# Kernel optimization log

Measured on AMD Instinct MI355X. Metric: run time of the kernel, lower is better.

## Reference

```python
import jax, jax.numpy as jnp
import numpy as np

EPS = 1e-6
NUM_HEADS = 12


def setup_inputs() -> dict:
    key = jax.random.key(0)
    k1, k2, k3, k4 = jax.random.split(key, 4)
    B, N, C = 8, 1024, 768
    x = jax.random.normal(k1, (B, N, C), dtype=jnp.float32)
    # random-walk visitation mask (nonnegative, row 'start_node' weights)
    mask = jax.random.uniform(k2, (N, N), dtype=jnp.float32)
    w_qkv = jax.random.normal(k3, (C, 3 * C), dtype=jnp.float32) * (C ** -0.5)
    w_out = jax.random.normal(k4, (C, C), dtype=jnp.float32) * (C ** -0.5)
    b_out = jnp.zeros((C,), dtype=jnp.float32)
    return {"x": x, "mask": mask, "w_qkv": w_qkv, "w_out": w_out, "b_out": b_out}


def reference(x, mask, w_qkv, w_out, b_out):
    B, N, C = x.shape
    H = NUM_HEADS
    D = C // H
    qkv = x @ w_qkv                      # [B, N, 3C]
    q, k, v = jnp.split(qkv, 3, axis=-1)
    # [B, N, C] -> [B, H, N, D]
    to_heads = lambda t: t.reshape(B, N, H, D).transpose(0, 2, 1, 3)
    q, k, v = to_heads(q), to_heads(k), to_heads(v)
    # feature map: relu + eps
    q = jax.nn.relu(q) + EPS
    k = jax.nn.relu(k) + EPS
    # graph smoothing: (q^T @ mask)^T  ==  einsum over the token axis
    q_graph = jnp.einsum('bhnd,nm->bhmd', q, mask)
    k_graph = jnp.einsum('bhnd,nm->bhmd', k, mask)
    q = q + 0.1 * q_graph
    k = k + 0.1 * k_graph
    # exact linear kernel, masked by random-walk mask
    linear_kernel = jnp.einsum('bhnd,bhmd->bhnm', q, k)   # [B, H, N, N]
    masked_kernel = linear_kernel * mask[None, None]
    z = 1.0 / (masked_kernel.sum(axis=-1, keepdims=True) + EPS)
    out = jnp.einsum('bhnm,bhmd->bhnd', masked_kernel, v) * z
    out = out.transpose(0, 2, 1, 3).reshape(B, N, C)
    return out @ w_out + b_out
```

## Files before the change

kernel.cpp:

```cpp
#include <hip/hip_runtime.h>


typedef unsigned short u16;
typedef unsigned int u32;
typedef __attribute__((ext_vector_type(8))) short short8;
typedef __attribute__((ext_vector_type(4))) float f32x4;

#define MFMA(a, b, c) __builtin_amdgcn_mfma_f32_16x16x32_bf16((a), (b), (c), 0, 0, 0)

__device__ __forceinline__ u16 f2b(float f) {
    unsigned u = __builtin_bit_cast(unsigned, f);
    return (u16)((u + 0x7FFFu + ((u >> 16) & 1u)) >> 16);
}
__device__ __forceinline__ float b2f(u16 h) {
    unsigned u = ((unsigned)h) << 16;
    return __builtin_bit_cast(float, u);
}
__device__ __forceinline__ void gl_lds16(const u16* g, u16* l) {
    __builtin_amdgcn_global_load_lds(
        (const __attribute__((address_space(1))) u32*)g,
        (__attribute__((address_space(3))) u32*)l, 16, 0, 0);
}

__global__ __launch_bounds__(256) void k_conv(const float* __restrict__ in,
                                              u16* __restrict__ out, int n) {
    int i = (blockIdx.x * 256 + threadIdx.x) * 4;
    if (i + 3 < n) {
        float4 v = *reinterpret_cast<const float4*>(&in[i]);
        ushort4 o;
        o.x = f2b(v.x); o.y = f2b(v.y); o.z = f2b(v.z); o.w = f2b(v.w);
        *reinterpret_cast<ushort4*>(&out[i]) = o;
    }
}

__global__ __launch_bounds__(256) void k_transconv(const float* __restrict__ in,
                                                   u16* __restrict__ out,
                                                   int R, int Cc, float alpha, float delta) {
    __shared__ float t[32][33];
    const int tx = threadIdx.x & 31, ty = threadIdx.x >> 5;
    const int r0 = blockIdx.y * 32, c0 = blockIdx.x * 32;
#pragma unroll
    for (int k = 0; k < 4; ++k)
        t[ty + 8 * k][tx] = in[(long)(r0 + ty + 8 * k) * Cc + c0 + tx];
    __syncthreads();
#pragma unroll
    for (int k = 0; k < 4; ++k) {
        const int c = c0 + ty + 8 * k, r = r0 + tx;
        float v = t[tx][ty + 8 * k] * alpha + ((r == c) ? delta : 0.f);
        out[(long)c * R + r] = f2b(v);
    }
}

template <int MODE>
__global__ __launch_bounds__(256) void k_gemm(const u16* __restrict__ A,
                                              const u16* __restrict__ Bm,
                                              void* __restrict__ Cv,
                                              const float* __restrict__ bias,
                                              int M, int N, int K,
                                              int lda, int ldb, int ldc,
                                              long boffB, long boffC) {
    __shared__ u16 As[128][40];
    __shared__ u16 Bs[128][40];
    const int tid = threadIdx.x;
    const int lane = tid & 63, wid = tid >> 6;
    const int lo = lane & 15, hi = lane >> 4;
    const int wr = wid >> 1, wc = wid & 1;
    const int m0 = blockIdx.y * 128, n0 = blockIdx.x * 128;
    const u16* Bz = Bm + (long)blockIdx.z * boffB;
    const int srow = tid >> 1, skoff = (tid & 1) * 16;
    const u16* Ag = A + (long)(m0 + srow) * lda + skoff;
    const u16* Bg = Bz + (long)(n0 + srow) * ldb + skoff;

    f32x4 acc[4][4] = {};
    for (int k0 = 0; k0 < K; k0 += 32) {
        short8 a0 = *reinterpret_cast<const short8*>(Ag + k0);
        short8 a1 = *reinterpret_cast<const short8*>(Ag + k0 + 8);
        short8 b0 = *reinterpret_cast<const short8*>(Bg + k0);
        short8 b1 = *reinterpret_cast<const short8*>(Bg + k0 + 8);
        __syncthreads();
        *reinterpret_cast<short8*>(&As[srow][skoff]) = a0;
        *reinterpret_cast<short8*>(&As[srow][skoff + 8]) = a1;
        *reinterpret_cast<short8*>(&Bs[srow][skoff]) = b0;
        *reinterpret_cast<short8*>(&Bs[srow][skoff + 8]) = b1;
        __syncthreads();
        short8 af[4], bf_[4];
#pragma unroll
        for (int i = 0; i < 4; ++i)
            af[i] = *reinterpret_cast<const short8*>(&As[wr * 64 + i * 16 + lo][hi * 8]);
#pragma unroll
        for (int j = 0; j < 4; ++j)
            bf_[j] = *reinterpret_cast<const short8*>(&Bs[wc * 64 + j * 16 + lo][hi * 8]);
#pragma unroll
        for (int i = 0; i < 4; ++i)
#pragma unroll
            for (int j = 0; j < 4; ++j)
                acc[i][j] = MFMA(af[i], bf_[j], acc[i][j]);
    }

#pragma unroll
    for (int i = 0; i < 4; ++i)
#pragma unroll
        for (int j = 0; j < 4; ++j)
#pragma unroll
            for (int r = 0; r < 4; ++r) {
                const int m = m0 + wr * 64 + i * 16 + hi * 4 + r;
                const int n = n0 + wc * 64 + j * 16 + lo;
                float v = acc[i][j][r];
                if (MODE == 0) {
                    if (m < 1536) v = fmaxf(v, 0.f) + 1e-6f;
                    ((u16*)Cv)[(long)m * ldc + n] = f2b(v);
                } else if (MODE == 1) {
                    u16* Cz = (u16*)Cv + (long)blockIdx.z * boffC;
                    Cz[(long)m * ldc + n] = f2b(v);
                } else {
                    ((float*)Cv)[(long)m * ldc + n] = v + bias[n];
                }
            }
}

__global__ __launch_bounds__(256) void k_attn2(const u16* __restrict__ qks,
                                               const u16* __restrict__ qkvT,
                                               const u16* __restrict__ mb,
                                               u16* __restrict__ attn) {
    __shared__ u16 Ks[2][64][64];
    __shared__ u16 Vt[2][64][64];
    __shared__ u16 Sb[4][16][72];
    __shared__ float Zs[4][2][16];
    const int tid = threadIdx.x, wid = tid >> 6, lane = tid & 63;
    const int lo = lane & 15, hi = lane >> 4;
    const int n0 = blockIdx.x * 128;
    const int bh = blockIdx.y, b = bh / 12, h = bh % 12;
    const long qbase = (long)b * 1024 * 1536;

    short8 aq[2][2];
#pragma unroll
    for (int qg = 0; qg < 2; ++qg)
#pragma unroll
        for (int kd = 0; kd < 2; ++kd)
            aq[qg][kd] = *reinterpret_cast<const short8*>(
                &qks[qbase + (long)(n0 + wid * 32 + qg * 16 + lo) * 1536 + h * 64 +
                     kd * 32 + hi * 8]);

    const u16* gK[2];
    const u16* gV[2];
    int ldsrow[2];
#pragma unroll
    for (int i = 0; i < 2; ++i) {
        const int r = wid * 16 + i * 8 + (lane >> 3);
        const int cs = (lane & 7) ^ (r & 7);
        ldsrow[i] = wid * 16 + i * 8;
        gK[i] = qks + qbase + (long)r * 1536 + 768 + h * 64 + cs * 8;
        gV[i] = qkvT + (long)(1536 + h * 64 + r) * 8192 + (long)b * 1024 + cs * 8;
    }

    const u16* mrow[2];
#pragma unroll
    for (int qg = 0; qg < 2; ++qg)
        mrow[qg] = mb + (long)(n0 + wid * 32 + qg * 16 + lo) * 1024;

    f32x4 oacc[2][4] = {};
    float rsum[2] = {0.f, 0.f};

#pragma unroll
    for (int i = 0; i < 2; ++i) {
        gl_lds16(gK[i], &Ks[0][ldsrow[i]][0]);
        gl_lds16(gV[i], &Vt[0][ldsrow[i]][0]);
    }
    __syncthreads();

    for (int t = 0; t < 16; ++t) {
        const int cur = t & 1;
        if (t < 15) {
            const long m1 = (long)(t + 1) * 64;
#pragma unroll
            for (int i = 0; i < 2; ++i) {
                gl_lds16(gK[i] + m1 * 1536, &Ks[cur ^ 1][ldsrow[i]][0]);
                gl_lds16(gV[i] + m1, &Vt[cur ^ 1][ldsrow[i]][0]);
            }
        }
        short8 kfr[4][2];
#pragma unroll
        for (int jm = 0; jm < 4; ++jm)
#pragma unroll
            for (int kd = 0; kd < 2; ++kd)
                kfr[jm][kd] = *reinterpret_cast<const short8*>(
                    &Ks[cur][jm * 16 + lo][(((kd * 4 + hi) ^ (lo & 7))) * 8]);

#pragma unroll
        for (int qg = 0; qg < 2; ++qg) {
            f32x4 s[4];
#pragma unroll
            for (int jm = 0; jm < 4; ++jm) {
                f32x4 sj = {};
                sj = MFMA(kfr[jm][0], aq[qg][0], sj);
                sj = MFMA(kfr[jm][1], aq[qg][1], sj);
                s[jm] = sj;
            }
#pragma unroll
            for (int jm = 0; jm < 4; ++jm) {
                ushort4 mv = *reinterpret_cast<const ushort4*>(
                    &mrow[qg][t * 64 + jm * 16 + hi * 4]);
                const u16 h0 = f2b(s[jm][0] * b2f(mv.x));
                const u16 h1 = f2b(s[jm][1] * b2f(mv.y));
                const u16 h2 = f2b(s[jm][2] * b2f(mv.z));
                const u16 h3 = f2b(s[jm][3] * b2f(mv.w));
                rsum[qg] += (b2f(h0) + b2f(h1)) + (b2f(h2) + b2f(h3));
                uint2 packed;
                packed.x = (u32)h0 | ((u32)h1 << 16);
                packed.y = (u32)h2 | ((u32)h3 << 16);
                *reinterpret_cast<uint2*>(&Sb[wid][lo][jm * 16 + hi * 4]) = packed;
            }
#pragma unroll
            for (int km = 0; km < 2; ++km) {
                const short8 pa =
                    *reinterpret_cast<const short8*>(&Sb[wid][lo][km * 32 + hi * 8]);
#pragma unroll
                for (int jd = 0; jd < 4; ++jd) {
                    const short8 vfr = *reinterpret_cast<const short8*>(
                        &Vt[cur][jd * 16 + lo][(((km * 4 + hi) ^ (lo & 7))) * 8]);
                    oacc[qg][jd] = MFMA(pa, vfr, oacc[qg][jd]);
                }
            }
        }
        __syncthreads();
    }

#pragma unroll
    for (int qg = 0; qg < 2; ++qg) {
        float v = rsum[qg];
        v += __shfl_xor(v, 16);
        v += __shfl_xor(v, 32);
        if (hi == 0) Zs[wid][qg][lo] = 1.f / (v + 1e-6f);
    }
    const long obase = (long)(b * 1024) * 768 + h * 64;
#pragma unroll
    for (int qg = 0; qg < 2; ++qg)
#pragma unroll
        for (int jd = 0; jd < 4; ++jd)
#pragma unroll
            for (int r = 0; r < 4; ++r) {
                const int nr = n0 + wid * 32 + qg * 16 + hi * 4 + r;
                attn[obase + (long)nr * 768 + jd * 16 + lo] =
                    f2b(oacc[qg][jd][r] * Zs[wid][qg][hi * 4 + r]);
            }
}


extern "C" void kernel_launch(void* const* d_in, const int* in_sizes, int n_in,
                              void* d_out, int out_size, void* d_ws, size_t ws_size,
                              hipStream_t stream) {
    (void)in_sizes; (void)n_in; (void)out_size; (void)ws_size;
    const float* x     = (const float*)d_in[0];
    const float* mask  = (const float*)d_in[1];
    const float* w_qkv = (const float*)d_in[2];
    const float* w_out = (const float*)d_in[3];
    const float* b_out = (const float*)d_in[4];
    float* out = (float*)d_out;

    u16* ws = (u16*)d_ws;
    u16* xb     = ws;
    u16* wqkvT  = xb + (size_t)8192 * 768;
    u16* mTb    = wqkvT + (size_t)2304 * 768;
    u16* woutT  = mTb + (size_t)1024 * 1024;
    u16* qkvT   = woutT + (size_t)768 * 768;
    u16* qks    = qkvT + (size_t)2304 * 8192;
    u16* attnb  = qks + (size_t)8192 * 1536;
    u16* mbb    = attnb + (size_t)8192 * 768;

    k_conv<<<dim3(6144), dim3(256), 0, stream>>>(x, xb, 8192 * 768);
    k_conv<<<dim3(1024), dim3(256), 0, stream>>>(mask, mbb, 1024 * 1024);
    k_transconv<<<dim3(72, 24), dim3(256), 0, stream>>>(w_qkv, wqkvT, 768, 2304, 1.f, 0.f);
    k_transconv<<<dim3(32, 32), dim3(256), 0, stream>>>(mask, mTb, 1024, 1024, 0.1f, 1.f);
    k_transconv<<<dim3(24, 24), dim3(256), 0, stream>>>(w_out, woutT, 768, 768, 1.f, 0.f);

    k_gemm<0><<<dim3(64, 18, 1), dim3(256), 0, stream>>>(
        wqkvT, xb, qkvT, nullptr, 2304, 8192, 768, 768, 768, 8192, 0, 0);
    k_gemm<1><<<dim3(12, 8, 8), dim3(256), 0, stream>>>(
        mTb, qkvT, qks, nullptr, 1024, 1536, 1024, 1024, 8192, 1536,
        1024L, 1024L * 1536L);
    k_attn2<<<dim3(8, 96), dim3(256), 0, stream>>>(qks, qkvT, mbb, attnb);
    k_gemm<2><<<dim3(6, 64, 1), dim3(256), 0, stream>>>(
        attnb, woutT, out, b_out, 8192, 768, 768, 768, 768, 768, 0, 0);
}
```

Baseline: 273.2 us.

## Load GEMM tiles via direct global-to-LDS and pack bf16 with hardware convert

The generic GEMM now stages A and B tiles with global_load_lds, going straight into unpadded 32-wide shared arrays. This replaces register-staged loads followed by LDS stores. In the attention kernel, the masked scores are packed to bf16 with v_cvt_pk_bf16_f32 rather than manual rounding, and the row sum is accumulated from the unrounded fp32 products. Dropping the row padding may add LDS bank conflicts on fragment reads. The row-sum change slightly alters numerics.

Result: faster. 266.0 us (-2.7%).

```diff
diff --git a/kernel.cpp b/kernel.cpp
--- a/kernel.cpp
+++ b/kernel.cpp
@@ -15,6 +15,11 @@
 __device__ __forceinline__ float b2f(u16 h) {
     unsigned u = ((unsigned)h) << 16;
     return __builtin_bit_cast(float, u);
+}
+__device__ __forceinline__ u32 cvt_pk_bf16(float a, float b) {
+    u32 r;
+    asm("v_cvt_pk_bf16_f32 %0, %1, %2" : "=v"(r) : "v"(a), "v"(b));
+    return r;
 }
 __device__ __forceinline__ void gl_lds16(const u16* g, u16* l) {
     __builtin_amdgcn_global_load_lds(
@@ -59,37 +64,38 @@
                                               int M, int N, int K,
                                               int lda, int ldb, int ldc,
                                               long boffB, long boffC) {
-    __shared__ u16 As[128][40];
-    __shared__ u16 Bs[128][40];
+    __shared__ u16 As[128 * 32];
+    __shared__ u16 Bs[128 * 32];
     const int tid = threadIdx.x;
     const int lane = tid & 63, wid = tid >> 6;
     const int lo = lane & 15, hi = lane >> 4;
     const int wr = wid >> 1, wc = wid & 1;
     const int m0 = blockIdx.y * 128, n0 = blockIdx.x * 128;
     const u16* Bz = Bm + (long)blockIdx.z * boffB;
-    const int srow = tid >> 1, skoff = (tid & 1) * 16;
-    const u16* Ag = A + (long)(m0 + srow) * lda + skoff;
-    const u16* Bg = Bz + (long)(n0 + srow) * ldb + skoff;
+
+    const int rA = wid * 32 + (lane >> 2);
+    const int ck = (lane & 3) * 8;
+    const u16* Ag = A + (long)(m0 + rA) * lda + ck;
+    const u16* Bg = Bz + (long)(n0 + rA) * ldb + ck;
+    u16* AsW = As + (wid * 32) * 32;
+    u16* BsW = Bs + (wid * 32) * 32;
 
     f32x4 acc[4][4] = {};
     for (int k0 = 0; k0 < K; k0 += 32) {
-        short8 a0 = *reinterpret_cast<const short8*>(Ag + k0);
-        short8 a1 = *reinterpret_cast<const short8*>(Ag + k0 + 8);
-        short8 b0 = *reinterpret_cast<const short8*>(Bg + k0);
-        short8 b1 = *reinterpret_cast<const short8*>(Bg + k0 + 8);
         __syncthreads();
-        *reinterpret_cast<short8*>(&As[srow][skoff]) = a0;
-        *reinterpret_cast<short8*>(&As[srow][skoff + 8]) = a1;
-        *reinterpret_cast<short8*>(&Bs[srow][skoff]) = b0;
-        *reinterpret_cast<short8*>(&Bs[srow][skoff + 8]) = b1;
+#pragma unroll
+        for (int i = 0; i < 2; ++i) {
+            gl_lds16(Ag + (long)i * 16 * lda + k0, AsW + i * 16 * 32);
+            gl_lds16(Bg + (long)i * 16 * ldb + k0, BsW + i * 16 * 32);
+        }
         __syncthreads();
         short8 af[4], bf_[4];
 #pragma unroll
         for (int i = 0; i < 4; ++i)
-            af[i] = *reinterpret_cast<const short8*>(&As[wr * 64 + i * 16 + lo][hi * 8]);
+            af[i] = *reinterpret_cast<const short8*>(&As[(wr * 64 + i * 16 + lo) * 32 + hi * 8]);
 #pragma unroll
         for (int j = 0; j < 4; ++j)
-            bf_[j] = *reinterpret_cast<const short8*>(&Bs[wc * 64 + j * 16 + lo][hi * 8]);
+            bf_[j] = *reinterpret_cast<const short8*>(&Bs[(wc * 64 + j * 16 + lo) * 32 + hi * 8]);
 #pragma unroll
         for (int i = 0; i < 4; ++i)
 #pragma unroll
@@ -200,14 +206,14 @@
             for (int jm = 0; jm < 4; ++jm) {
                 ushort4 mv = *reinterpret_cast<const ushort4*>(
                     &mrow[qg][t * 64 + jm * 16 + hi * 4]);
-                const u16 h0 = f2b(s[jm][0] * b2f(mv.x));
-                const u16 h1 = f2b(s[jm][1] * b2f(mv.y));
-                const u16 h2 = f2b(s[jm][2] * b2f(mv.z));
-                const u16 h3 = f2b(s[jm][3] * b2f(mv.w));
-                rsum[qg] += (b2f(h0) + b2f(h1)) + (b2f(h2) + b2f(h3));
+                const float p0 = s[jm][0] * b2f(mv.x);
+                const float p1 = s[jm][1] * b2f(mv.y);
+                const float p2 = s[jm][2] * b2f(mv.z);
+                const float p3 = s[jm][3] * b2f(mv.w);
+                rsum[qg] += (p0 + p1) + (p2 + p3);
                 uint2 packed;
-                packed.x = (u32)h0 | ((u32)h1 << 16);
-                packed.y = (u32)h2 | ((u32)h3 << 16);
+                packed.x = cvt_pk_bf16(p0, p1);
+                packed.y = cvt_pk_bf16(p2, p3);
                 *reinterpret_cast<uint2*>(&Sb[wid][lo][jm * 16 + hi * 4]) = packed;
             }
 #pragma unroll
```
